# Optimization experiments

Hardware: AMD Instinct MI355X
Metric: run time of the kernel (lower is better)

The kernel has to match this reference:

```python
import jax, jax.numpy as jnp
import numpy as np

B, T, C, H = 4, 1024, 1024, 16
D = C // H  # head dim = 64


def setup_inputs() -> dict:
    key = jax.random.key(0)
    ks = jax.random.split(key, 12)
    s = 1.0 / np.sqrt(C)
    inp = {
        "x": jax.random.normal(ks[0], (B, T, C), jnp.float32),
        "Wq": jax.random.normal(ks[1], (C, C), jnp.float32) * s,
        "bq": jnp.zeros((C,), jnp.float32),
        "Wk": jax.random.normal(ks[2], (C, C), jnp.float32) * s,
        "bk": jnp.zeros((C,), jnp.float32),
        "Wv": jax.random.normal(ks[3], (C, C), jnp.float32) * s,
        "bv": jnp.zeros((C,), jnp.float32),
        "time_weighting": jnp.ones((H, T, T), jnp.float32),
        "head_mix_w": jax.random.normal(ks[4], (H, H), jnp.float32) * (1.0 / np.sqrt(H)),
        "Wp": jax.random.normal(ks[5], (C, C), jnp.float32) * s,
        "bp": jnp.zeros((C,), jnp.float32),
    }
    return inp


def reference(x, Wq, bq, Wk, bk, Wv, bv, time_weighting, head_mix_w, Wp, bp):
    Bx, Tx, Cx = x.shape
    half = Cx // 2
    # time_shift: first half of channels sees x shifted by one step (row 0 -> zeros)
    x_shift = jnp.pad(x, ((0, 0), (1, 0), (0, 0)))[:, :Tx, :half]
    xs = jnp.concatenate([x_shift, x[:, :, half:]], axis=-1)

    def heads(y):  # [B,T,C] -> [B,H,T,D]
        return y.reshape(Bx, Tx, H, D).transpose(0, 2, 1, 3)

    q = heads(xs @ Wq.T + bq)
    k = heads(xs @ Wk.T + bk)
    v = heads(xs @ Wv.T + bv)

    att = jnp.einsum("bhtd,bhsd->bhts", q, k) * (1.0 / np.sqrt(D))
    causal = jnp.tril(jnp.ones((Tx, Tx), bool))
    att = jnp.where(causal, att, -jnp.inf)
    att = jax.nn.softmax(att, axis=-1)
    att = att * time_weighting[:, :Tx, :Tx]
    # 1x1 conv across heads
    att = jnp.einsum("oh,bhts->bots", head_mix_w, att)

    y = jnp.einsum("bhts,bhsd->bhtd", att, v)
    y = y.transpose(0, 2, 1, 3).reshape(Bx, Tx, Cx)
    return y @ Wp.T + bp
```

## Files before the change

kernel.cpp:

```cpp
#include <hip/hip_runtime.h>
#include <hip/hip_bf16.h>

#define T_ 1024

typedef __attribute__((ext_vector_type(8))) short short8;
typedef __attribute__((ext_vector_type(4))) float f32x4;
typedef __bf16 bf16x8 __attribute__((ext_vector_type(8)));
typedef _Float16 f16x8 __attribute__((ext_vector_type(8)));
typedef __attribute__((ext_vector_type(4))) unsigned short ushort4v;

__device__ __forceinline__ unsigned short f2bf(float f) {
    unsigned u = __float_as_uint(f);
    u += 0x7fffu + ((u >> 16) & 1u);
    return (unsigned short)(u >> 16);
}
__device__ __forceinline__ float bf2f(unsigned short s) {
    return __uint_as_float(((unsigned)s) << 16);
}
__device__ __forceinline__ unsigned short f2h(float f) {
    _Float16 h = (_Float16)f;
    return __builtin_bit_cast(unsigned short, h);
}
__device__ __forceinline__ float h2f(unsigned short u) {
    return (float)__builtin_bit_cast(_Float16, u);
}

__global__ __launch_bounds__(256) void k_convert(
    const float* __restrict__ s0, const float* __restrict__ s1,
    const float* __restrict__ s2, const float* __restrict__ s3,
    unsigned short* __restrict__ d0, unsigned short* __restrict__ d1,
    unsigned short* __restrict__ d2, unsigned short* __restrict__ d3) {
    const float* src; unsigned short* dst;
    switch (blockIdx.y) {
        case 0:  src = s0; dst = d0; break;
        case 1:  src = s1; dst = d1; break;
        case 2:  src = s2; dst = d2; break;
        default: src = s3; dst = d3; break;
    }
    int i = (blockIdx.x * 256 + threadIdx.x) * 4;
    float4 v = *(const float4*)(src + i);
    ushort4v ov = { f2bf(v.x), f2bf(v.y), f2bf(v.z), f2bf(v.w) };
    *(ushort4v*)(dst + i) = ov;
}

__global__ __launch_bounds__(256) void k_xs(const float* __restrict__ x,
                                            unsigned short* __restrict__ xs) {
    int idx = (blockIdx.x * 256 + threadIdx.x) * 4;
    int c = idx & 1023;
    int m = idx >> 10;
    int t = m & 1023;
    float4 v;
    if (c < 512) {
        if (t == 0) { v.x = v.y = v.z = v.w = 0.f; }
        else        { v = *(const float4*)(x + (size_t)(m - 1) * 1024 + c); }
    } else {
        v = *(const float4*)(x + (size_t)m * 1024 + c);
    }
    ushort4v ov = { f2bf(v.x), f2bf(v.y), f2bf(v.z), f2bf(v.w) };
    *(ushort4v*)(xs + (size_t)m * 1024 + c) = ov;
}

__device__ __forceinline__ void gemm_body(const unsigned short* __restrict__ A,
                                          const unsigned short* __restrict__ Bt,
                                          int m0, int n0, int tid, f32x4 acc[4][4],
                                          unsigned short (*As)[32], unsigned short (*Bs)[32]) {
    const int lane = tid & 63, w = tid >> 6;
    const int wr = w >> 1, wc = w & 1;
#pragma unroll
    for (int i = 0; i < 4; i++)
#pragma unroll
        for (int j = 0; j < 4; j++) acc[i][j] = (f32x4){0.f, 0.f, 0.f, 0.f};

    for (int k0 = 0; k0 < 1024; k0 += 32) {
        __syncthreads();
#pragma unroll
        for (int it = 0; it < 2; it++) {
            int ch = it * 256 + tid;
            int row = ch >> 2, c = ch & 3;
            int col = (c ^ ((row >> 1) & 3)) * 8;
            *(short8*)&As[row][col] = *(const short8*)(A + (size_t)(m0 + row) * 1024 + k0 + c * 8);
            *(short8*)&Bs[row][col] = *(const short8*)(Bt + (size_t)(n0 + row) * 1024 + k0 + c * 8);
        }
        __syncthreads();
        bf16x8 af[4], bg[4];
        int c = lane >> 4;
#pragma unroll
        for (int i = 0; i < 4; i++) {
            int row = wr * 64 + i * 16 + (lane & 15);
            af[i] = *(const bf16x8*)&As[row][(c ^ ((row >> 1) & 3)) * 8];
        }
#pragma unroll
        for (int j = 0; j < 4; j++) {
            int row = wc * 64 + j * 16 + (lane & 15);
            bg[j] = *(const bf16x8*)&Bs[row][(c ^ ((row >> 1) & 3)) * 8];
        }
#pragma unroll
        for (int i = 0; i < 4; i++)
#pragma unroll
            for (int j = 0; j < 4; j++)
                acc[i][j] = __builtin_amdgcn_mfma_f32_16x16x32_bf16(af[i], bg[j], acc[i][j], 0, 0, 0);
    }
}

__global__ __launch_bounds__(256) void k_gemm_qkv(
    const unsigned short* __restrict__ A,
    const unsigned short* __restrict__ wq, const unsigned short* __restrict__ wk,
    const unsigned short* __restrict__ wv,
    const float* __restrict__ bq, const float* __restrict__ bk, const float* __restrict__ bv,
    unsigned short* __restrict__ qo, unsigned short* __restrict__ ko,
    unsigned short* __restrict__ vo) {
    __shared__ unsigned short As[128][32];
    __shared__ unsigned short Bs[128][32];
    const int mat = blockIdx.y >> 3;
    const unsigned short* Bt = mat == 0 ? wq : (mat == 1 ? wk : wv);
    const float* bias = mat == 0 ? bq : (mat == 1 ? bk : bv);
    unsigned short* out = mat == 0 ? qo : (mat == 1 ? ko : vo);
    const int m0 = blockIdx.x * 128, n0 = (blockIdx.y & 7) * 128;
    const int tid = threadIdx.x, lane = tid & 63, w = tid >> 6;
    const int wr = w >> 1, wc = w & 1;
    f32x4 acc[4][4];
    gemm_body(A, Bt, m0, n0, tid, acc, As, Bs);
#pragma unroll
    for (int i = 0; i < 4; i++) {
        int mbase = m0 + wr * 64 + i * 16 + ((lane >> 4) << 2);
#pragma unroll
        for (int j = 0; j < 4; j++) {
            int n = n0 + wc * 64 + j * 16 + (lane & 15);
            float bv_ = bias[n];
            int h = n >> 6, d = n & 63;
#pragma unroll
            for (int r = 0; r < 4; r++) {
                int mm = mbase + r;
                int b = mm >> 10, t = mm & 1023;
                out[(size_t)((b * 16 + h) * 1024 + t) * 64 + d] = f2bf(acc[i][j][r] + bv_);
            }
        }
    }
}

__global__ __launch_bounds__(256) void k_gemm_out(
    const unsigned short* __restrict__ A, const unsigned short* __restrict__ Bt,
    const float* __restrict__ bias, float* __restrict__ out) {
    __shared__ unsigned short As[128][32];
    __shared__ unsigned short Bs[128][32];
    const int m0 = blockIdx.x * 128, n0 = blockIdx.y * 128;
    const int tid = threadIdx.x, lane = tid & 63, w = tid >> 6;
    const int wr = w >> 1, wc = w & 1;
    f32x4 acc[4][4];
    gemm_body(A, Bt, m0, n0, tid, acc, As, Bs);
#pragma unroll
    for (int i = 0; i < 4; i++) {
        int mbase = m0 + wr * 64 + i * 16 + ((lane >> 4) << 2);
#pragma unroll
        for (int j = 0; j < 4; j++) {
            int n = n0 + wc * 64 + j * 16 + (lane & 15);
            float bv_ = bias[n];
#pragma unroll
            for (int r = 0; r < 4; r++)
                out[(size_t)(mbase + r) * 1024 + n] = acc[i][j][r] + bv_;
        }
    }
}

__global__ __launch_bounds__(256) void k_scores(const unsigned short* __restrict__ qb,
                                                const unsigned short* __restrict__ kb,
                                                unsigned short* __restrict__ Eb,
                                                float* __restrict__ invb) {
    __shared__ unsigned short qs[64][64];
    __shared__ unsigned short ks[64][64];
    const int tid = threadIdx.x, lane = tid & 63, w = tid >> 6;
    const int t0 = (15 - (int)blockIdx.x) * 64;
    const int bh = blockIdx.y;
    const unsigned short* qp = qb + (size_t)bh * 65536;
    const unsigned short* kp = kb + (size_t)bh * 65536;

#pragma unroll
    for (int it = 0; it < 2; it++) {
        int ch = it * 256 + tid; int row = ch >> 3, c = ch & 7;
        *(short8*)&qs[row][(c ^ (row & 7)) * 8] = *(const short8*)(qp + (size_t)(t0 + row) * 64 + c * 8);
    }
    __syncthreads();
    const int row_a = w * 16 + (lane & 15);
    bf16x8 a0 = *(const bf16x8*)&qs[row_a][(((lane >> 4)    ) ^ (row_a & 7)) * 8];
    bf16x8 a1 = *(const bf16x8*)&qs[row_a][(((lane >> 4) + 4) ^ (row_a & 7)) * 8];
    const int tr = t0 + w * 16 + ((lane >> 4) << 2);
    float l_[4] = {0.f, 0.f, 0.f, 0.f};
    unsigned short* ep = Eb + (size_t)bh * ((size_t)T_ * T_);

    for (int s0 = 0; s0 <= t0 + 63; s0 += 64) {
        __syncthreads();
#pragma unroll
        for (int it = 0; it < 2; it++) {
            int ch = it * 256 + tid; int row = ch >> 3, c = ch & 7;
            *(short8*)&ks[row][(c ^ (row & 7)) * 8] = *(const short8*)(kp + (size_t)(s0 + row) * 64 + c * 8);
        }
        __syncthreads();
        f32x4 S[4];
#pragma unroll
        for (int sf = 0; sf < 4; sf++) {
            int row = sf * 16 + (lane & 15);
            bf16x8 b0 = *(const bf16x8*)&ks[row][(((lane >> 4)    ) ^ (row & 7)) * 8];
            bf16x8 b1 = *(const bf16x8*)&ks[row][(((lane >> 4) + 4) ^ (row & 7)) * 8];
            f32x4 z = (f32x4){0.f, 0.f, 0.f, 0.f};
            z = __builtin_amdgcn_mfma_f32_16x16x32_bf16(a0, b0, z, 0, 0, 0);
            z = __builtin_amdgcn_mfma_f32_16x16x32_bf16(a1, b1, z, 0, 0, 0);
            S[sf] = z;
        }
#pragma unroll
        for (int sf = 0; sf < 4; sf++) {
            int s = s0 + sf * 16 + (lane & 15);
#pragma unroll
            for (int r = 0; r < 4; r++) {
                float es = (s <= tr + r) ? __expf(S[sf][r] * 0.125f) : 0.f;
                l_[r] += es;
                ep[(size_t)(tr + r) * T_ + s] = f2h(es);
            }
        }
    }
#pragma unroll
    for (int r = 0; r < 4; r++) {
        float ts = l_[r];
        ts += __shfl_xor(ts, 1);
        ts += __shfl_xor(ts, 2);
        ts += __shfl_xor(ts, 4);
        ts += __shfl_xor(ts, 8);
        l_[r] = ts;
    }
    if ((lane & 15) == 0) {
#pragma unroll
        for (int r = 0; r < 4; r++) invb[(size_t)bh * T_ + tr + r] = 1.f / l_[r];
    }
}

__global__ __launch_bounds__(256) void k_mix2(unsigned short* __restrict__ Sb,
                                              const float* __restrict__ invb,
                                              const float* __restrict__ tw,
                                              const float* __restrict__ mixw) {
    const int t = blockIdx.y, b = blockIdx.z;
    const int send = t | 63;
    if ((int)(blockIdx.x * 256) > send) return;
    const int tid = threadIdx.x, lane = tid & 63, w = tid >> 6;
    const int s = blockIdx.x * 256 + tid;
    __shared__ unsigned short p2[256][32];
    __shared__ float inv_s[16];
    if (tid < 16) inv_s[tid] = invb[(size_t)(b * 16 + tid) * T_ + t];
    __syncthreads();

    const bool live = (s <= send);
    unsigned rowbase = (unsigned)t * 1024u + (unsigned)s;
    unsigned short* plane0 = Sb + (size_t)b * 16 * 1048576;
    short8 lo, hi;
#pragma unroll
    for (int hh = 0; hh < 8; hh++) {
        float e0 = 0.f, e1 = 0.f;
        if (live) {
            e0 = h2f(plane0[(size_t)hh * 1048576 + rowbase]) * inv_s[hh]
                 * tw[(size_t)hh * 1048576 + rowbase];
            e1 = h2f(plane0[(size_t)(hh + 8) * 1048576 + rowbase]) * inv_s[hh + 8]
                 * tw[(size_t)(hh + 8) * 1048576 + rowbase];
        }
        ((unsigned short*)&lo)[hh] = f2h(e0);
        ((unsigned short*)&hi)[hh] = f2h(e1);
    }
    short8 zz = {0, 0, 0, 0, 0, 0, 0, 0};
    int sw = (tid >> 1) & 3;
    *(short8*)&p2[tid][(0 ^ sw) * 8] = lo;
    *(short8*)&p2[tid][(1 ^ sw) * 8] = hi;
    *(short8*)&p2[tid][(2 ^ sw) * 8] = zz;
    *(short8*)&p2[tid][(3 ^ sw) * 8] = zz;

    short8 afb;
#pragma unroll
    for (int j = 0; j < 8; j++) {
        int k = (lane >> 4) * 8 + j;
        float mv = (k < 16) ? mixw[(lane & 15) * 16 + k] : 0.f;
        ((unsigned short*)&afb)[j] = f2h(mv);
    }
    f16x8 af = __builtin_bit_cast(f16x8, afb);
    __syncthreads();

#pragma unroll
    for (int g = 0; g < 4; g++) {
        int pos = (w * 4 + g) * 16 + (lane & 15);
        f16x8 bf = *(const f16x8*)&p2[pos][(((lane >> 4)) ^ ((pos >> 1) & 3)) * 8];
        f32x4 d = (f32x4){0.f, 0.f, 0.f, 0.f};
        d = __builtin_amdgcn_mfma_f32_16x16x32_f16(af, bf, d, 0, 0, 0);
        int spos = blockIdx.x * 256 + pos;
        if (spos <= send) {
            unsigned ob = (unsigned)t * 1024u + (unsigned)spos;
#pragma unroll
            for (int r = 0; r < 4; r++) {
                int o = (lane >> 4) * 4 + r;
                plane0[(size_t)o * 1048576 + ob] = f2bf(d[r]);
            }
        }
    }
}

__global__ __launch_bounds__(256) void k_av(const unsigned short* __restrict__ att,
                                            const unsigned short* __restrict__ vb,
                                            unsigned short* __restrict__ y1) {
    __shared__ unsigned short as_[64][64];
    __shared__ unsigned short vs[64][72];
    const int tid = threadIdx.x, lane = tid & 63, w = tid >> 6;
    const int t0 = (15 - (int)blockIdx.x) * 64;
    const int bh = blockIdx.y;
    const int b = bh >> 4, h = bh & 15;
    const unsigned short* ap = att + (size_t)bh * 1048576;
    const unsigned short* vp = vb + (size_t)bh * 65536;
    f32x4 acc[4];
#pragma unroll
    for (int j = 0; j < 4; j++) acc[j] = (f32x4){0.f, 0.f, 0.f, 0.f};

    for (int s0 = 0; s0 <= t0 + 63; s0 += 64) {
        __syncthreads();
#pragma unroll
        for (int it = 0; it < 2; it++) {
            int ch = it * 256 + tid;
            int row = ch >> 3, c = ch & 7;
            *(short8*)&as_[row][(c ^ (row & 7)) * 8] =
                *(const short8*)(ap + (size_t)(t0 + row) * 1024 + s0 + c * 8);
            int sp = ch >> 3, dc = (ch & 7) * 8;
            short8 vv = *(const short8*)(vp + (size_t)(s0 + sp) * 64 + dc);
#pragma unroll
            for (int i = 0; i < 8; i++) vs[dc + i][sp] = ((unsigned short*)&vv)[i];
        }
        __syncthreads();
        const int row_a = w * 16 + (lane & 15);
#pragma unroll
        for (int ks = 0; ks < 2; ks++) {
            bf16x8 af = *(const bf16x8*)&as_[row_a][((((lane >> 4) + 4 * ks)) ^ (row_a & 7)) * 8];
#pragma unroll
            for (int j = 0; j < 4; j++) {
                bf16x8 bg = *(const bf16x8*)&vs[j * 16 + (lane & 15)][ks * 32 + (lane >> 4) * 8];
                acc[j] = __builtin_amdgcn_mfma_f32_16x16x32_bf16(af, bg, acc[j], 0, 0, 0);
            }
        }
    }

    int t = t0 + w * 16 + ((lane >> 4) << 2);
#pragma unroll
    for (int j = 0; j < 4; j++) {
        int d = j * 16 + (lane & 15);
#pragma unroll
        for (int r = 0; r < 4; r++)
            y1[(size_t)(b * 1024 + t + r) * 1024 + h * 64 + d] = f2bf(acc[j][r]);
    }
}

extern "C" void kernel_launch(void* const* d_in, const int* in_sizes, int n_in,
                              void* d_out, int out_size, void* d_ws, size_t ws_size,
                              hipStream_t stream) {
    (void)in_sizes; (void)n_in; (void)out_size; (void)ws_size;
    const float* x    = (const float*)d_in[0];
    const float* Wq   = (const float*)d_in[1];
    const float* bq   = (const float*)d_in[2];
    const float* Wk   = (const float*)d_in[3];
    const float* bk   = (const float*)d_in[4];
    const float* Wv   = (const float*)d_in[5];
    const float* bv   = (const float*)d_in[6];
    const float* tw   = (const float*)d_in[7];
    const float* mixw = (const float*)d_in[8];
    const float* Wp   = (const float*)d_in[9];
    const float* bp   = (const float*)d_in[10];

    char* ws = (char*)d_ws;
    size_t off = 0;
    auto alloc = [&](size_t bytes) -> char* {
        char* p = ws + off;
        off += (bytes + 255) & ~(size_t)255;
        return p;
    };
    unsigned short* xs  = (unsigned short*)alloc((size_t)4096 * 1024 * 2);
    unsigned short* wqb = (unsigned short*)alloc((size_t)1024 * 1024 * 2);
    unsigned short* wkb = (unsigned short*)alloc((size_t)1024 * 1024 * 2);
    unsigned short* wvb = (unsigned short*)alloc((size_t)1024 * 1024 * 2);
    unsigned short* wpb = (unsigned short*)alloc((size_t)1024 * 1024 * 2);
    unsigned short* qb  = (unsigned short*)alloc((size_t)64 * 1024 * 64 * 2);
    unsigned short* kb  = (unsigned short*)alloc((size_t)64 * 1024 * 64 * 2);
    unsigned short* vb_ = (unsigned short*)alloc((size_t)64 * 1024 * 64 * 2);
    unsigned short* Sb  = (unsigned short*)alloc((size_t)64 * 1024 * 1024 * 2);
    float*          invb = (float*)alloc((size_t)64 * 1024 * 4);
    unsigned short* y1  = (unsigned short*)alloc((size_t)4096 * 1024 * 2);

    k_convert<<<dim3(1024, 4), 256, 0, stream>>>(Wq, Wk, Wv, Wp, wqb, wkb, wvb, wpb);
    k_xs<<<4096, 256, 0, stream>>>(x, xs);
    k_gemm_qkv<<<dim3(32, 24), 256, 0, stream>>>(xs, wqb, wkb, wvb, bq, bk, bv, qb, kb, vb_);
    k_scores<<<dim3(16, 64), 256, 0, stream>>>(qb, kb, Sb, invb);
    k_mix2<<<dim3(4, 1024, 4), 256, 0, stream>>>(Sb, invb, tw, mixw);
    k_av<<<dim3(16, 64), 256, 0, stream>>>(Sb, vb_, y1);
    k_gemm_out<<<dim3(32, 8), 256, 0, stream>>>(y1, wpb, bp, (float*)d_out);
}
```

Baseline: 368.8 us.

## Process full attention row per block in head-mix kernel with vectorized loads

```diff
diff --git a/kernel.cpp b/kernel.cpp
--- a/kernel.cpp
+++ b/kernel.cpp
@@ -7,6 +7,7 @@
 typedef __attribute__((ext_vector_type(4))) float f32x4;
 typedef __bf16 bf16x8 __attribute__((ext_vector_type(8)));
 typedef _Float16 f16x8 __attribute__((ext_vector_type(8)));
+typedef _Float16 f16x4 __attribute__((ext_vector_type(4)));
 typedef __attribute__((ext_vector_type(4))) unsigned short ushort4v;
 
 __device__ __forceinline__ unsigned short f2bf(float f) {
@@ -232,67 +233,56 @@
     }
 }
 
-__global__ __launch_bounds__(256) void k_mix2(unsigned short* __restrict__ Sb,
+__global__ __launch_bounds__(256) void k_mix3(unsigned short* __restrict__ Sb,
                                               const float* __restrict__ invb,
                                               const float* __restrict__ tw,
                                               const float* __restrict__ mixw) {
-    const int t = blockIdx.y, b = blockIdx.z;
+    const int t = blockIdx.x, b = blockIdx.y;
     const int send = t | 63;
-    if ((int)(blockIdx.x * 256) > send) return;
-    const int tid = threadIdx.x, lane = tid & 63, w = tid >> 6;
-    const int s = blockIdx.x * 256 + tid;
-    __shared__ unsigned short p2[256][32];
+    const int tid = threadIdx.x, lane = tid & 63, w = tid >> 6;
+    __shared__ unsigned short p2[1024][24];
     __shared__ float inv_s[16];
     if (tid < 16) inv_s[tid] = invb[(size_t)(b * 16 + tid) * T_ + t];
     __syncthreads();
 
-    const bool live = (s <= send);
-    unsigned rowbase = (unsigned)t * 1024u + (unsigned)s;
     unsigned short* plane0 = Sb + (size_t)b * 16 * 1048576;
-    short8 lo, hi;
-#pragma unroll
-    for (int hh = 0; hh < 8; hh++) {
-        float e0 = 0.f, e1 = 0.f;
-        if (live) {
-            e0 = h2f(plane0[(size_t)hh * 1048576 + rowbase]) * inv_s[hh]
-                 * tw[(size_t)hh * 1048576 + rowbase];
-            e1 = h2f(plane0[(size_t)(hh + 8) * 1048576 + rowbase]) * inv_s[hh + 8]
-                 * tw[(size_t)(hh + 8) * 1048576 + rowbase];
-        }
-        ((unsigned short*)&lo)[hh] = f2h(e0);
-        ((unsigned short*)&hi)[hh] = f2h(e1);
-    }
-    short8 zz = {0, 0, 0, 0, 0, 0, 0, 0};
-    int sw = (tid >> 1) & 3;
-    *(short8*)&p2[tid][(0 ^ sw) * 8] = lo;
-    *(short8*)&p2[tid][(1 ^ sw) * 8] = hi;
-    *(short8*)&p2[tid][(2 ^ sw) * 8] = zz;
-    *(short8*)&p2[tid][(3 ^ sw) * 8] = zz;
-
-    short8 afb;
-#pragma unroll
-    for (int j = 0; j < 8; j++) {
-        int k = (lane >> 4) * 8 + j;
-        float mv = (k < 16) ? mixw[(lane & 15) * 16 + k] : 0.f;
-        ((unsigned short*)&afb)[j] = f2h(mv);
-    }
-    f16x8 af = __builtin_bit_cast(f16x8, afb);
+    const int s4 = tid * 4;
+    if (s4 <= send) {
+        const unsigned rowb = (unsigned)t * 1024u + (unsigned)s4;
+        unsigned short ph[4][16];
+#pragma unroll
+        for (int h = 0; h < 16; h++) {
+            ushort4v e4 = *(const ushort4v*)(plane0 + (size_t)h * 1048576 + rowb);
+            float4 t4 = *(const float4*)(tw + (size_t)h * 1048576 + rowb);
+            float iv = inv_s[h];
+            ph[0][h] = f2h(h2f(e4.x) * iv * t4.x);
+            ph[1][h] = f2h(h2f(e4.y) * iv * t4.y);
+            ph[2][h] = f2h(h2f(e4.z) * iv * t4.z);
+            ph[3][h] = f2h(h2f(e4.w) * iv * t4.w);
+        }
+#pragma unroll
+        for (int j = 0; j < 4; j++) {
+            *(short8*)&p2[s4 + j][0] = *(short8*)&ph[j][0];
+            *(short8*)&p2[s4 + j][8] = *(short8*)&ph[j][8];
+        }
+    }
+
+    f16x4 af;
+#pragma unroll
+    for (int j = 0; j < 4; j++)
+        af[j] = (_Float16)mixw[(lane & 15) * 16 + (lane >> 4) * 4 + j];
     __syncthreads();
 
-#pragma unroll
-    for (int g = 0; g < 4; g++) {
-        int pos = (w * 4 + g) * 16 + (lane & 15);
-        f16x8 bf = *(const f16x8*)&p2[pos][(((lane >> 4)) ^ ((pos >> 1) & 3)) * 8];
-        f32x4 d = (f32x4){0.f, 0.f, 0.f, 0.f};
-        d = __builtin_amdgcn_mfma_f32_16x16x32_f16(af, bf, d, 0, 0, 0);
-        int spos = blockIdx.x * 256 + pos;
-        if (spos <= send) {
-            unsigned ob = (unsigned)t * 1024u + (unsigned)spos;
-#pragma unroll
-            for (int r = 0; r < 4; r++) {
-                int o = (lane >> 4) * 4 + r;
-                plane0[(size_t)o * 1048576 + ob] = f2bf(d[r]);
-            }
+    const int ng = (send + 1) >> 4;
+    const unsigned obase = (unsigned)t * 1024u;
+    for (int g = w; g < ng; g += 4) {
+        int pos = g * 16 + (lane & 15);
+        f16x4 bf = *(const f16x4*)&p2[pos][(lane >> 4) * 4];
+        f32x4 d = __builtin_amdgcn_mfma_f32_16x16x16f16(af, bf, (f32x4){0.f, 0.f, 0.f, 0.f}, 0, 0, 0);
+#pragma unroll
+        for (int r = 0; r < 4; r++) {
+            int o = (lane >> 4) * 4 + r;
+            plane0[(size_t)o * 1048576 + obase + pos] = f2bf(d[r]);
         }
     }
 }
@@ -387,7 +377,7 @@
     k_xs<<<4096, 256, 0, stream>>>(x, xs);
     k_gemm_qkv<<<dim3(32, 24), 256, 0, stream>>>(xs, wqb, wkb, wvb, bq, bk, bv, qb, kb, vb_);
     k_scores<<<dim3(16, 64), 256, 0, stream>>>(qb, kb, Sb, invb);
-    k_mix2<<<dim3(4, 1024, 4), 256, 0, stream>>>(Sb, invb, tw, mixw);
+    k_mix3<<<dim3(1024, 4), 256, 0, stream>>>(Sb, invb, tw, mixw);
     k_av<<<dim3(16, 64), 256, 0, stream>>>(Sb, vb_, y1);
     k_gemm_out<<<dim3(32, 8), 256, 0, stream>>>(y1, wpb, bp, (float*)d_out);
 }
```

Result: faster. 333.9 us (-9.5%).
